# Performance work log

Hardware: AMD Instinct MI355X
Metric: run time of the kernel (lower is better)

Reference implementation:

```python
import jax, jax.numpy as jnp
import numpy as np
import math

D_MODEL = 512
N_HEADS = 8
D_K = D_MODEL // N_HEADS
N_SAMPLES = 16
BETA = 1.0
SCALE = 1.0 / math.sqrt(D_K)
PROPOSAL_TEMP = 0.5


def setup_inputs() -> dict:
    key = jax.random.key(0)
    ks = jax.random.split(key, 9)
    B, S = 2, 512
    x = jax.random.normal(ks[0], (B, S, D_MODEL), dtype=jnp.float32)
    init = lambda k: jax.random.normal(k, (D_MODEL, D_MODEL), dtype=jnp.float32) * 0.02
    return {
        "x": x,
        "Wq": init(ks[1]), "bq": jnp.zeros((D_MODEL,), jnp.float32),
        "Wk": init(ks[2]), "bk": jnp.zeros((D_MODEL,), jnp.float32),
        "Wv": init(ks[3]), "bv": jnp.zeros((D_MODEL,), jnp.float32),
        "Wo": init(ks[4]), "bo": jnp.zeros((D_MODEL,), jnp.float32),
    }


def _importance_sampled_weights(scores):
    # scores: [B,H,S,S]. Replicates the per-row Python loop, fully vectorized.
    B, H, Sq, Sk = scores.shape
    target = jax.nn.softmax(scores * BETA, axis=-1)            # [B,H,Sq,Sk]
    # optimal proposal: 0.5*target + 0.5*uniform
    prop = PROPOSAL_TEMP * target + (1.0 - PROPOSAL_TEMP) / Sk
    R = B * H * Sq
    tf = target.reshape(R, Sk)
    pf = prop.reshape(R, Sk)
    # tsu_backend.sample_binary_layer(log(p/(1-p))) == Bernoulli(p) sampling
    s = jax.random.bernoulli(jax.random.key(42), pf[:, None, :], (R, N_SAMPLES, Sk))
    # importance weight = prod(target[sel]) / (prod(prop[sel]) * prod(1-prop[~sel]))
    pt = jnp.prod(jnp.where(s, tf[:, None, :], 1.0), axis=-1)                 # [R,N]
    pp = jnp.prod(jnp.where(s, pf[:, None, :], 1.0 - pf[:, None, :]), axis=-1)
    valid = (s.sum(-1) > 0) & (pp > 0)
    w = jnp.where(valid, pt / jnp.maximum(pp, 1e-38), 0.0)
    ws = w.sum(-1, keepdims=True)
    w = jnp.where(ws > 0, w / jnp.maximum(ws, 1e-38), 1.0 / N_SAMPLES)        # [R,N]
    wa = jnp.einsum('rn,rnk->rk', w, s.astype(jnp.float32))                   # [R,Sk]
    was = wa.sum(-1, keepdims=True)
    wa = jnp.where(was > 0, wa / jnp.maximum(was, 1e-38), 1.0 / Sk)
    return wa.reshape(B, H, Sq, Sk)


def reference(x, Wq, bq, Wk, bk, Wv, bv, Wo, bo):
    B, S, Dm = x.shape
    proj = lambda W, b: (x @ W + b).reshape(B, S, N_HEADS, D_K).transpose(0, 2, 1, 3)
    Q = proj(Wq, bq)  # [B,H,S,dk]
    K = proj(Wk, bk)
    V = proj(Wv, bv)
    scores = jnp.einsum('bhqd,bhkd->bhqk', Q, K) * SCALE
    # torch builds weights via torch.tensor(...) which detaches => constant w.r.t. params
    attn = jax.lax.stop_gradient(_importance_sampled_weights(scores))
    out = jnp.einsum('bhqk,bhkd->bhqd', attn, V)
    out = out.transpose(0, 2, 1, 3).reshape(B, S, Dm)
    return out @ Wo + bo
```

## Files before the change

### kernel.cpp

```cpp
#include <hip/hip_runtime.h>
#include <cstdint>
#include <cstddef>


#define ROTL(x, r) __builtin_rotateleft32((x), (r))

#define QR8(s)                                                                \
  x0[0]+=x1[0];x0[1]+=x1[1];x0[2]+=x1[2];x0[3]+=x1[3];                        \
  x0[4]+=x1[4];x0[5]+=x1[5];x0[6]+=x1[6];x0[7]+=x1[7];                        \
  x1[0]=ROTL(x1[0],s);x1[1]=ROTL(x1[1],s);x1[2]=ROTL(x1[2],s);                \
  x1[3]=ROTL(x1[3],s);x1[4]=ROTL(x1[4],s);x1[5]=ROTL(x1[5],s);                \
  x1[6]=ROTL(x1[6],s);x1[7]=ROTL(x1[7],s);                                    \
  x1[0]^=x0[0];x1[1]^=x0[1];x1[2]^=x0[2];x1[3]^=x0[3];                        \
  x1[4]^=x0[4];x1[5]^=x0[5];x1[6]^=x0[6];x1[7]^=x0[7];
#define INJ8(X, Y)                                                            \
  x0[0]+=(X);x0[1]+=(X);x0[2]+=(X);x0[3]+=(X);                                \
  x0[4]+=(X);x0[5]+=(X);x0[6]+=(X);x0[7]+=(X);                                \
  x1[0]+=(Y);x1[1]+=(Y);x1[2]+=(Y);x1[3]+=(Y);                                \
  x1[4]+=(Y);x1[5]+=(Y);x1[6]+=(Y);x1[7]+=(Y);
#define INJ8Y(Y)                                                              \
  x1[0]+=(Y);x1[1]+=(Y);x1[2]+=(Y);x1[3]+=(Y);                                \
  x1[4]+=(Y);x1[5]+=(Y);x1[6]+=(Y);x1[7]+=(Y);

__global__ __launch_bounds__(256)
void qkv_gemm(const float* __restrict__ x,
              const float* __restrict__ Wq, const float* __restrict__ bq,
              const float* __restrict__ Wk, const float* __restrict__ bk,
              const float* __restrict__ Wv, const float* __restrict__ bv,
              const float* __restrict__ bo, float* __restrict__ outp,
              float* __restrict__ Qw, float* __restrict__ KTw,
              float* __restrict__ Vw) {
  const int tid = threadIdx.x;
  if (blockIdx.z == 3) {
    const int blk = blockIdx.y * 16 + blockIdx.x;
    const size_t base4 = (size_t)blk * 1024 + tid;
    const float4* bo4 = (const float4*)bo;
    float4* out4 = (float4*)outp;
#pragma unroll
    for (int i = 0; i < 4; ++i) {
      const size_t idx4 = base4 + (size_t)i * 256;
      out4[idx4] = bo4[idx4 & 127];
    }
    return;
  }
  const float* W; const float* bias;
  if (blockIdx.z == 0)      { W = Wq; bias = bq; }
  else if (blockIdx.z == 1) { W = Wk; bias = bk; }
  else                      { W = Wv; bias = bv; }

  __shared__ __align__(16) float smem[64 * 68];
  float (*At)[68] = (float(*)[68])smem;
  float (*Bs)[64] = (float(*)[64])(smem + 32 * 68);
  float (*T2)[68] = (float(*)[68])smem;

  const int tx = tid & 15, ty = tid >> 4;
  const int row0 = blockIdx.x * 64, col0 = blockIdx.y * 64;
  float acc[4][4] = {};

  const int ar = tid >> 2;
  const int kc0 = (tid & 3) << 3;
  const int br0 = tid >> 4,         bc0 = (tid & 15) << 2;
  const int br1 = (tid + 256) >> 4, bc1 = ((tid + 256) & 15) << 2;

  float4 aReg0, aReg1, bReg0, bReg1;
  {
    const int kk = 0;
    aReg0 = *(const float4*)&x[(size_t)(row0 + ar) * 512 + kk + kc0];
    aReg1 = *(const float4*)&x[(size_t)(row0 + ar) * 512 + kk + kc0 + 4];
    bReg0 = *(const float4*)&W[(size_t)(kk + br0) * 512 + col0 + bc0];
    bReg1 = *(const float4*)&W[(size_t)(kk + br1) * 512 + col0 + bc1];
  }

  for (int kk = 0; kk < 512; kk += 32) {
    At[kc0 + 0][ar] = aReg0.x; At[kc0 + 1][ar] = aReg0.y;
    At[kc0 + 2][ar] = aReg0.z; At[kc0 + 3][ar] = aReg0.w;
    At[kc0 + 4][ar] = aReg1.x; At[kc0 + 5][ar] = aReg1.y;
    At[kc0 + 6][ar] = aReg1.z; At[kc0 + 7][ar] = aReg1.w;
    *(float4*)&Bs[br0][bc0] = bReg0;
    *(float4*)&Bs[br1][bc1] = bReg1;
    __syncthreads();
    if (kk < 480) {
      const int kn = kk + 32;
      aReg0 = *(const float4*)&x[(size_t)(row0 + ar) * 512 + kn + kc0];
      aReg1 = *(const float4*)&x[(size_t)(row0 + ar) * 512 + kn + kc0 + 4];
      bReg0 = *(const float4*)&W[(size_t)(kn + br0) * 512 + col0 + bc0];
      bReg1 = *(const float4*)&W[(size_t)(kn + br1) * 512 + col0 + bc1];
    }
#pragma unroll
    for (int p = 0; p < 32; ++p) {
      const float4 a4 = *(const float4*)&At[p][ty << 2];
      const float4 b4 = *(const float4*)&Bs[p][tx << 2];
      acc[0][0] = fmaf(a4.x, b4.x, acc[0][0]); acc[0][1] = fmaf(a4.x, b4.y, acc[0][1]);
      acc[0][2] = fmaf(a4.x, b4.z, acc[0][2]); acc[0][3] = fmaf(a4.x, b4.w, acc[0][3]);
      acc[1][0] = fmaf(a4.y, b4.x, acc[1][0]); acc[1][1] = fmaf(a4.y, b4.y, acc[1][1]);
      acc[1][2] = fmaf(a4.y, b4.z, acc[1][2]); acc[1][3] = fmaf(a4.y, b4.w, acc[1][3]);
      acc[2][0] = fmaf(a4.z, b4.x, acc[2][0]); acc[2][1] = fmaf(a4.z, b4.y, acc[2][1]);
      acc[2][2] = fmaf(a4.z, b4.z, acc[2][2]); acc[2][3] = fmaf(a4.z, b4.w, acc[2][3]);
      acc[3][0] = fmaf(a4.w, b4.x, acc[3][0]); acc[3][1] = fmaf(a4.w, b4.y, acc[3][1]);
      acc[3][2] = fmaf(a4.w, b4.z, acc[3][2]); acc[3][3] = fmaf(a4.w, b4.w, acc[3][3]);
    }
    __syncthreads();
  }

  if (blockIdx.z == 0) {
#pragma unroll
    for (int i = 0; i < 4; ++i) {
      const int row = row0 + (ty << 2) + i;
      const int b = row >> 9, s = row & 511;
#pragma unroll
      for (int j = 0; j < 4; ++j) {
        const int col = col0 + (tx << 2) + j;
        const int h = col >> 6, d = col & 63;
        Qw[(((size_t)(b * 8 + h) * 512 + s) * 64) + d] = acc[i][j] + bias[col];
      }
    }
  } else if (blockIdx.z == 1) {
#pragma unroll
    for (int i = 0; i < 4; ++i) {
#pragma unroll
      for (int j = 0; j < 4; ++j) {
        const int col = col0 + (tx << 2) + j;
        T2[(tx << 2) + j][(ty << 2) + i] = acc[i][j] + bias[col];
      }
    }
    __syncthreads();
    const int c = tid >> 2, seg = tid & 3;
    const int b = row0 >> 9, h = blockIdx.y;
    const int s0 = (row0 & 511) + (seg << 4);
    float* dst = KTw + (((size_t)(b * 8 + h) * 64 + c) << 9) + s0;
#pragma unroll
    for (int i2 = 0; i2 < 4; ++i2) {
      *(float4*)&dst[i2 << 2] = *(const float4*)&T2[c][(seg << 4) + (i2 << 2)];
    }
  } else {
#pragma unroll
    for (int i = 0; i < 4; ++i) {
      const int row = row0 + (ty << 2) + i;
      const int b = row >> 9, s = row & 511;
#pragma unroll
      for (int j = 0; j < 4; ++j) {
        const int col = col0 + (tx << 2) + j;
        const int h = col >> 6, d = col & 63;
        Vw[(((size_t)(b * 8 + h) * 512 + s) * 64) + d] = acc[i][j] + bias[col];
      }
    }
  }
}

__global__ __launch_bounds__(256)
void fused_sample(const float* __restrict__ Q, const float* __restrict__ KT,
                  const float* __restrict__ V, const float* __restrict__ Wo,
                  float* __restrict__ outp) {
  const int bx = blockIdx.x;
  const int rbase = ((((bx & 7) << 8) | (bx >> 3)) << 2);
  const int bh = rbase >> 9, q0 = rbase & 511;
  const int b = rbase >> 12, h = (rbase >> 9) & 7;
  const int tid = threadIdx.x;

  __shared__ __align__(16) float qs[4][64];
  __shared__ __align__(16) float scs[4][512];
  __shared__ float red[8];
  __shared__ float redc[8];
  __shared__ float wr[16];
  __shared__ float tf[512];
  __shared__ __align__(16) uint32_t pscu2[512];
  __shared__ float wa[512];
  __shared__ float psum[4][64];
  __shared__ __align__(16) float o_s[4][64];
  __shared__ int   list[512];
  __shared__ int   cnt;

  qs[tid >> 6][tid & 63] =
      Q[((size_t)bh * 512 + q0 + (tid >> 6)) * 64 + (tid & 63)];
  __syncthreads();

  {
    const float* Kp = KT + (size_t)bh * 64 * 512 + tid;
    float s00 = 0.f, s01 = 0.f, s10 = 0.f, s11 = 0.f;
    float s20 = 0.f, s21 = 0.f, s30 = 0.f, s31 = 0.f;
#pragma unroll
    for (int d4 = 0; d4 < 16; ++d4) {
      float k0v[4], k1v[4];
#pragma unroll
      for (int j = 0; j < 4; ++j) {
        k0v[j] = Kp[(size_t)(d4 * 4 + j) * 512];
        k1v[j] = Kp[(size_t)(d4 * 4 + j) * 512 + 256];
      }
      const float4 q0v = *(const float4*)&qs[0][d4 << 2];
      const float4 q1v = *(const float4*)&qs[1][d4 << 2];
      const float4 q2v = *(const float4*)&qs[2][d4 << 2];
      const float4 q3v = *(const float4*)&qs[3][d4 << 2];
      s00 = fmaf(q0v.x, k0v[0], s00); s00 = fmaf(q0v.y, k0v[1], s00);
      s00 = fmaf(q0v.z, k0v[2], s00); s00 = fmaf(q0v.w, k0v[3], s00);
      s01 = fmaf(q0v.x, k1v[0], s01); s01 = fmaf(q0v.y, k1v[1], s01);
      s01 = fmaf(q0v.z, k1v[2], s01); s01 = fmaf(q0v.w, k1v[3], s01);
      s10 = fmaf(q1v.x, k0v[0], s10); s10 = fmaf(q1v.y, k0v[1], s10);
      s10 = fmaf(q1v.z, k0v[2], s10); s10 = fmaf(q1v.w, k0v[3], s10);
      s11 = fmaf(q1v.x, k1v[0], s11); s11 = fmaf(q1v.y, k1v[1], s11);
      s11 = fmaf(q1v.z, k1v[2], s11); s11 = fmaf(q1v.w, k1v[3], s11);
      s20 = fmaf(q2v.x, k0v[0], s20); s20 = fmaf(q2v.y, k0v[1], s20);
      s20 = fmaf(q2v.z, k0v[2], s20); s20 = fmaf(q2v.w, k0v[3], s20);
      s21 = fmaf(q2v.x, k1v[0], s21); s21 = fmaf(q2v.y, k1v[1], s21);
      s21 = fmaf(q2v.z, k1v[2], s21); s21 = fmaf(q2v.w, k1v[3], s21);
      s30 = fmaf(q3v.x, k0v[0], s30); s30 = fmaf(q3v.y, k0v[1], s30);
      s30 = fmaf(q3v.z, k0v[2], s30); s30 = fmaf(q3v.w, k0v[3], s30);
      s31 = fmaf(q3v.x, k1v[0], s31); s31 = fmaf(q3v.y, k1v[1], s31);
      s31 = fmaf(q3v.z, k1v[2], s31); s31 = fmaf(q3v.w, k1v[3], s31);
    }
    scs[0][tid] = s00 * 0.125f; scs[0][tid + 256] = s01 * 0.125f;
    scs[1][tid] = s10 * 0.125f; scs[1][tid + 256] = s11 * 0.125f;
    scs[2][tid] = s20 * 0.125f; scs[2][tid + 256] = s21 * 0.125f;
    scs[3][tid] = s30 * 0.125f; scs[3][tid + 256] = s31 * 0.125f;
  }

  const int n = tid >> 4, t = tid & 15;
  const int k0i = t << 5;
  const int g = tid >> 6, d = tid & 63;
  const float* Vb = V + ((size_t)(b * 8 + h) * 512) * 64;

  for (int rr = 0; rr < 4; ++rr) {
    const int r = rbase + rr;
    const float sc0 = scs[rr][tid];
    const float sc1 = scs[rr][tid + 256];

    float mx = fmaxf(sc0, sc1);
    for (int m = 1; m < 64; m <<= 1) mx = fmaxf(mx, __shfl_xor(mx, m));
    if ((tid & 63) == 0) red[tid >> 6] = mx;
    __syncthreads();
    const float rowmax = fmaxf(fmaxf(red[0], red[1]), fmaxf(red[2], red[3]));
    const float e0 = expf(sc0 - rowmax);
    const float e1 = expf(sc1 - rowmax);
    float ssum = e0 + e1;
    for (int m = 1; m < 64; m <<= 1) ssum += __shfl_xor(ssum, m);
    if ((tid & 63) == 0) red[4 + (tid >> 6)] = ssum;
    if (tid == 0) cnt = 0;
    __syncthreads();
    const float tot = red[4] + red[5] + red[6] + red[7];
    const float t0 = e0 / tot, t1 = e1 / tot;
    tf[tid] = t0; tf[tid + 256] = t1;
    wa[tid] = 0.f; wa[tid + 256] = 0.f;
    {
      const float p0 = fmaf(0.5f, t0, 0.0009765625f);
      const float p1 = fmaf(0.5f, t1, 0.0009765625f);
      {
        const int k = tid;
        pscu2[(((k & 31) >> 2) << 6) + ((k >> 5) << 2) + (k & 3)] =
            ((uint32_t)ceilf(p0 * 8388608.0f)) << 9;
      }
      {
        const int k = tid + 256;
        pscu2[(((k & 31) >> 2) << 6) + ((k >> 5) << 2) + (k & 3)] =
            ((uint32_t)ceilf(p1 * 8388608.0f)) << 9;
      }
      float ql = (1.f - p0) * (1.f - p1);
      for (int m = 1; m < 64; m <<= 1) ql *= __shfl_xor(ql, m);
      if ((tid & 63) == 0) redc[4 + (tid >> 6)] = ql;
    }
    __syncthreads();
    const float Qrow = redc[4] * redc[5] * redc[6] * redc[7];

    const uint32_t cbase =
        (uint32_t)r * 8192u + (uint32_t)n * 512u + (uint32_t)k0i + 42u;
    uint32_t bits = 0u;
#pragma unroll
    for (int jb = 0; jb < 32; jb += 8) {
      uint32_t x0[8], x1[8];
#pragma unroll
      for (int i = 0; i < 8; ++i) {
        const uint32_t c = cbase + (uint32_t)(jb + i);
        x0[i] = c;
        x1[i] = ROTL(c, 13) ^ c;
      }
      QR8(15) QR8(26) QR8(6)
      INJ8(42u, 0x1BD11BF1u)
      QR8(17) QR8(29) QR8(16) QR8(24)
      INJ8(0x1BD11BF0u, 2u)
      QR8(13) QR8(15) QR8(26) QR8(6)
      INJ8Y(45u)
      QR8(17) QR8(29) QR8(16) QR8(24)
      INJ8(42u, 0x1BD11BF4u)
      QR8(13) QR8(15) QR8(26) QR8(6)
      INJ8(0x1BD11BF0u, 5u)
      const uint4 pA = *(const uint4*)&pscu2[((jb >> 2) << 6) + (t << 2)];
      const uint4 pB = *(const uint4*)&pscu2[(((jb >> 2) + 1) << 6) + (t << 2)];
      bits |= (uint32_t)((x0[0] ^ x1[0]) < pA.x) << (jb + 0);
      bits |= (uint32_t)((x0[1] ^ x1[1]) < pA.y) << (jb + 1);
      bits |= (uint32_t)((x0[2] ^ x1[2]) < pA.z) << (jb + 2);
      bits |= (uint32_t)((x0[3] ^ x1[3]) < pA.w) << (jb + 3);
      bits |= (uint32_t)((x0[4] ^ x1[4]) < pB.x) << (jb + 4);
      bits |= (uint32_t)((x0[5] ^ x1[5]) < pB.y) << (jb + 5);
      bits |= (uint32_t)((x0[6] ^ x1[6]) < pB.z) << (jb + 6);
      bits |= (uint32_t)((x0[7] ^ x1[7]) < pB.w) << (jb + 7);
    }

    float ptl = 1.f, ratl = 1.f;
    int cl = __popc(bits);
    {
      uint32_t bb = bits;
      while (bb) {
        const int j = __builtin_ctz(bb);
        bb &= bb - 1u;
        const float tv = tf[k0i + j];
        const float p = fmaf(0.5f, tv, 0.0009765625f);
        ptl *= tv;
        ratl *= p / (1.f - p);
      }
    }
#pragma unroll
    for (int m = 1; m < 16; m <<= 1) {
      ptl *= __shfl_xor(ptl, m);
      ratl *= __shfl_xor(ratl, m);
      cl += __shfl_xor(cl, m);
    }
    if (t == 0) {
      const float pp = Qrow * ratl;
      wr[n] = (cl > 0 && pp > 0.f) ? (ptl / fmaxf(pp, 1e-38f)) : 0.f;
    }
    __syncthreads();
    float wsum = 0.f;
#pragma unroll
    for (int m2 = 0; m2 < 16; ++m2) wsum += wr[m2];
    const float wn = (wsum > 0.f) ? (wr[n] / fmaxf(wsum, 1e-38f)) : 0.0625f;
    {
      uint32_t bb = bits;
      while (bb) {
        const int j = __builtin_ctz(bb);
        bb &= bb - 1u;
        atomicAdd(&wa[k0i + j], wn);
      }
    }
    __syncthreads();

    float sp = wa[tid] + wa[tid + 256];
    for (int m = 1; m < 64; m <<= 1) sp += __shfl_xor(sp, m);
    if ((tid & 63) == 0) redc[tid >> 6] = sp;
    if (wa[tid] > 0.f)       { const int i = atomicAdd(&cnt, 1); list[i] = tid; }
    if (wa[tid + 256] > 0.f) { const int i = atomicAdd(&cnt, 1); list[i] = tid + 256; }
    __syncthreads();
    const float was = redc[0] + redc[1] + redc[2] + redc[3];
    const int nnz = cnt;

    float acc = 0.f;
    if (was > 0.f) {
      const float inv = 1.f / fmaxf(was, 1e-38f);
      for (int i = g; i < nnz; i += 4) {
        const int k = list[i];
        acc = fmaf(wa[k] * inv, Vb[(size_t)k * 64 + d], acc);
      }
    } else {
      for (int k = g; k < 512; k += 4) acc += Vb[(size_t)k * 64 + d];
      acc *= 0.001953125f;
    }
    psum[g][d] = acc;
    __syncthreads();
    if (g == 0)
      o_s[rr][d] = psum[0][d] + psum[1][d] + psum[2][d] + psum[3][d];
  }
  __syncthreads();

  {
    const float* Wh = Wo + ((size_t)h * 64) * 512;
    float a00 = 0.f, a01 = 0.f, a10 = 0.f, a11 = 0.f;
    float a20 = 0.f, a21 = 0.f, a30 = 0.f, a31 = 0.f;
#pragma unroll 8
    for (int dd = 0; dd < 64; ++dd) {
      const float w0 = Wh[(size_t)dd * 512 + tid];
      const float w1 = Wh[(size_t)dd * 512 + tid + 256];
      const float o0 = o_s[0][dd], o1 = o_s[1][dd];
      const float o2 = o_s[2][dd], o3 = o_s[3][dd];
      a00 = fmaf(o0, w0, a00); a01 = fmaf(o0, w1, a01);
      a10 = fmaf(o1, w0, a10); a11 = fmaf(o1, w1, a11);
      a20 = fmaf(o2, w0, a20); a21 = fmaf(o2, w1, a21);
      a30 = fmaf(o3, w0, a30); a31 = fmaf(o3, w1, a31);
    }
    float* orow = outp + ((size_t)(b * 512 + q0)) * 512;
    atomicAdd(&orow[tid], a00);         atomicAdd(&orow[tid + 256], a01);
    atomicAdd(&orow[512 + tid], a10);   atomicAdd(&orow[512 + tid + 256], a11);
    atomicAdd(&orow[1024 + tid], a20);  atomicAdd(&orow[1024 + tid + 256], a21);
    atomicAdd(&orow[1536 + tid], a30);  atomicAdd(&orow[1536 + tid + 256], a31);
  }
}

extern "C" void kernel_launch(void* const* d_in, const int* in_sizes, int n_in,
                              void* d_out, int out_size, void* d_ws,
                              size_t ws_size, hipStream_t stream) {
  const float* x  = (const float*)d_in[0];
  const float* Wq = (const float*)d_in[1];
  const float* bq = (const float*)d_in[2];
  const float* Wk = (const float*)d_in[3];
  const float* bk = (const float*)d_in[4];
  const float* Wv = (const float*)d_in[5];
  const float* bv = (const float*)d_in[6];
  const float* Wo = (const float*)d_in[7];
  const float* bo = (const float*)d_in[8];
  float* out = (float*)d_out;

  float* ws = (float*)d_ws;
  float* Qw = ws;
  float* KT = ws + 524288;
  float* Vw = ws + 1048576;

  dim3 gq(16, 8, 4);
  qkv_gemm<<<gq, 256, 0, stream>>>(x, Wq, bq, Wk, bk, Wv, bv, bo, out,
                                   Qw, KT, Vw);
  fused_sample<<<2048, 256, 0, stream>>>(Qw, KT, Vw, Wo, out);
}
```

Baseline: 247.8 us.

## Halve QKV GEMM row tile and double-buffer shared memory tiles

The QKV projection GEMM now uses 32-row tiles instead of 64, doubling the grid to 1024 blocks for better occupancy across CUs. Shared memory A/B tiles are double-buffered so the next tile is stored while the current one is consumed, removing one barrier per k-step. Each thread now computes a 2x4 output block, which lowers arithmetic intensity per shared load. The bias-broadcast init blocks and K-transpose epilogue are adjusted to the new tile shape.

```diff
diff --git a/kernel.cpp b/kernel.cpp
--- a/kernel.cpp
+++ b/kernel.cpp
@@ -32,15 +32,12 @@
               float* __restrict__ Vw) {
   const int tid = threadIdx.x;
   if (blockIdx.z == 3) {
-    const int blk = blockIdx.y * 16 + blockIdx.x;
-    const size_t base4 = (size_t)blk * 1024 + tid;
+    const int blk = blockIdx.y * 32 + blockIdx.x;
+    const size_t base4 = (size_t)blk * 512 + tid;
     const float4* bo4 = (const float4*)bo;
     float4* out4 = (float4*)outp;
-#pragma unroll
-    for (int i = 0; i < 4; ++i) {
-      const size_t idx4 = base4 + (size_t)i * 256;
-      out4[idx4] = bo4[idx4 & 127];
-    }
+    out4[base4] = bo4[base4 & 127];
+    out4[base4 + 256] = bo4[(base4 + 256) & 127];
     return;
   }
   const float* W; const float* bias;
@@ -48,101 +45,95 @@
   else if (blockIdx.z == 1) { W = Wk; bias = bk; }
   else                      { W = Wv; bias = bv; }
 
-  __shared__ __align__(16) float smem[64 * 68];
-  float (*At)[68] = (float(*)[68])smem;
-  float (*Bs)[64] = (float(*)[64])(smem + 32 * 68);
-  float (*T2)[68] = (float(*)[68])smem;
+  __shared__ __align__(16) float smem[2 * (32 * 34 + 32 * 64)];
+  float (*At0)[34] = (float(*)[34])smem;
+  float (*Bs0)[64] = (float(*)[64])(smem + 32 * 34);
+  float (*At1)[34] = (float(*)[34])(smem + 3136);
+  float (*Bs1)[64] = (float(*)[64])(smem + 3136 + 32 * 34);
+  float (*T2)[34]  = (float(*)[34])smem;
 
   const int tx = tid & 15, ty = tid >> 4;
-  const int row0 = blockIdx.x * 64, col0 = blockIdx.y * 64;
-  float acc[4][4] = {};
-
-  const int ar = tid >> 2;
-  const int kc0 = (tid & 3) << 3;
+  const int row0 = blockIdx.x * 32, col0 = blockIdx.y * 64;
+  float acc[2][4] = {};
+
+  const int ar = tid >> 3;
+  const int kc = (tid & 7) << 2;
   const int br0 = tid >> 4,         bc0 = (tid & 15) << 2;
   const int br1 = (tid + 256) >> 4, bc1 = ((tid + 256) & 15) << 2;
 
-  float4 aReg0, aReg1, bReg0, bReg1;
-  {
-    const int kk = 0;
-    aReg0 = *(const float4*)&x[(size_t)(row0 + ar) * 512 + kk + kc0];
-    aReg1 = *(const float4*)&x[(size_t)(row0 + ar) * 512 + kk + kc0 + 4];
-    bReg0 = *(const float4*)&W[(size_t)(kk + br0) * 512 + col0 + bc0];
-    bReg1 = *(const float4*)&W[(size_t)(kk + br1) * 512 + col0 + bc1];
-  }
+  float4 aR, bR0, bR1;
+  aR  = *(const float4*)&x[(size_t)(row0 + ar) * 512 + kc];
+  bR0 = *(const float4*)&W[(size_t)br0 * 512 + col0 + bc0];
+  bR1 = *(const float4*)&W[(size_t)br1 * 512 + col0 + bc1];
+
+  At0[kc + 0][ar] = aR.x; At0[kc + 1][ar] = aR.y;
+  At0[kc + 2][ar] = aR.z; At0[kc + 3][ar] = aR.w;
+  *(float4*)&Bs0[br0][bc0] = bR0;
+  *(float4*)&Bs0[br1][bc1] = bR1;
+  __syncthreads();
+
+  float (*Atc)[34] = At0; float (*Bsc)[64] = Bs0;
+  float (*Atn)[34] = At1; float (*Bsn)[64] = Bs1;
 
   for (int kk = 0; kk < 512; kk += 32) {
-    At[kc0 + 0][ar] = aReg0.x; At[kc0 + 1][ar] = aReg0.y;
-    At[kc0 + 2][ar] = aReg0.z; At[kc0 + 3][ar] = aReg0.w;
-    At[kc0 + 4][ar] = aReg1.x; At[kc0 + 5][ar] = aReg1.y;
-    At[kc0 + 6][ar] = aReg1.z; At[kc0 + 7][ar] = aReg1.w;
-    *(float4*)&Bs[br0][bc0] = bReg0;
-    *(float4*)&Bs[br1][bc1] = bReg1;
-    __syncthreads();
     if (kk < 480) {
       const int kn = kk + 32;
-      aReg0 = *(const float4*)&x[(size_t)(row0 + ar) * 512 + kn + kc0];
-      aReg1 = *(const float4*)&x[(size_t)(row0 + ar) * 512 + kn + kc0 + 4];
-      bReg0 = *(const float4*)&W[(size_t)(kn + br0) * 512 + col0 + bc0];
-      bReg1 = *(const float4*)&W[(size_t)(kn + br1) * 512 + col0 + bc1];
+      aR  = *(const float4*)&x[(size_t)(row0 + ar) * 512 + kn + kc];
+      bR0 = *(const float4*)&W[(size_t)(kn + br0) * 512 + col0 + bc0];
+      bR1 = *(const float4*)&W[(size_t)(kn + br1) * 512 + col0 + bc1];
     }
 #pragma unroll
     for (int p = 0; p < 32; ++p) {
-      const float4 a4 = *(const float4*)&At[p][ty << 2];
-      const float4 b4 = *(const float4*)&Bs[p][tx << 2];
-      acc[0][0] = fmaf(a4.x, b4.x, acc[0][0]); acc[0][1] = fmaf(a4.x, b4.y, acc[0][1]);
-      acc[0][2] = fmaf(a4.x, b4.z, acc[0][2]); acc[0][3] = fmaf(a4.x, b4.w, acc[0][3]);
-      acc[1][0] = fmaf(a4.y, b4.x, acc[1][0]); acc[1][1] = fmaf(a4.y, b4.y, acc[1][1]);
-      acc[1][2] = fmaf(a4.y, b4.z, acc[1][2]); acc[1][3] = fmaf(a4.y, b4.w, acc[1][3]);
-      acc[2][0] = fmaf(a4.z, b4.x, acc[2][0]); acc[2][1] = fmaf(a4.z, b4.y, acc[2][1]);
-      acc[2][2] = fmaf(a4.z, b4.z, acc[2][2]); acc[2][3] = fmaf(a4.z, b4.w, acc[2][3]);
-      acc[3][0] = fmaf(a4.w, b4.x, acc[3][0]); acc[3][1] = fmaf(a4.w, b4.y, acc[3][1]);
-      acc[3][2] = fmaf(a4.w, b4.z, acc[3][2]); acc[3][3] = fmaf(a4.w, b4.w, acc[3][3]);
-    }
-    __syncthreads();
-  }
-
-  if (blockIdx.z == 0) {
-#pragma unroll
-    for (int i = 0; i < 4; ++i) {
-      const int row = row0 + (ty << 2) + i;
+      const float2 a2 = *(const float2*)&Atc[p][ty << 1];
+      const float4 b4 = *(const float4*)&Bsc[p][tx << 2];
+      acc[0][0] = fmaf(a2.x, b4.x, acc[0][0]); acc[0][1] = fmaf(a2.x, b4.y, acc[0][1]);
+      acc[0][2] = fmaf(a2.x, b4.z, acc[0][2]); acc[0][3] = fmaf(a2.x, b4.w, acc[0][3]);
+      acc[1][0] = fmaf(a2.y, b4.x, acc[1][0]); acc[1][1] = fmaf(a2.y, b4.y, acc[1][1]);
+      acc[1][2] = fmaf(a2.y, b4.z, acc[1][2]); acc[1][3] = fmaf(a2.y, b4.w, acc[1][3]);
+    }
+    if (kk < 480) {
+      Atn[kc + 0][ar] = aR.x; Atn[kc + 1][ar] = aR.y;
+      Atn[kc + 2][ar] = aR.z; Atn[kc + 3][ar] = aR.w;
+      *(float4*)&Bsn[br0][bc0] = bR0;
+      *(float4*)&Bsn[br1][bc1] = bR1;
+    }
+    __syncthreads();
+    float (*tA)[34] = Atc; Atc = Atn; Atn = tA;
+    float (*tB)[64] = Bsc; Bsc = Bsn; Bsn = tB;
+  }
+
+  const int h = blockIdx.y;
+  if (blockIdx.z == 0 || blockIdx.z == 2) {
+    float* dst = (blockIdx.z == 0) ? Qw : Vw;
+#pragma unroll
+    for (int i = 0; i < 2; ++i) {
+      const int row = row0 + (ty << 1) + i;
       const int b = row >> 9, s = row & 511;
 #pragma unroll
       for (int j = 0; j < 4; ++j) {
         const int col = col0 + (tx << 2) + j;
-        const int h = col >> 6, d = col & 63;
-        Qw[(((size_t)(b * 8 + h) * 512 + s) * 64) + d] = acc[i][j] + bias[col];
-      }
-    }
-  } else if (blockIdx.z == 1) {
-#pragma unroll
-    for (int i = 0; i < 4; ++i) {
+        const int d = col & 63;
+        dst[(((size_t)(b * 8 + h) * 512 + s) * 64) + d] = acc[i][j] + bias[col];
+      }
+    }
+  } else {
+#pragma unroll
+    for (int i = 0; i < 2; ++i) {
 #pragma unroll
       for (int j = 0; j < 4; ++j) {
         const int col = col0 + (tx << 2) + j;
-        T2[(tx << 2) + j][(ty << 2) + i] = acc[i][j] + bias[col];
-      }
-    }
-    __syncthreads();
-    const int c = tid >> 2, seg = tid & 3;
-    const int b = row0 >> 9, h = blockIdx.y;
-    const int s0 = (row0 & 511) + (seg << 4);
-    float* dst = KTw + (((size_t)(b * 8 + h) * 64 + c) << 9) + s0;
-#pragma unroll
-    for (int i2 = 0; i2 < 4; ++i2) {
-      *(float4*)&dst[i2 << 2] = *(const float4*)&T2[c][(seg << 4) + (i2 << 2)];
-    }
-  } else {
-#pragma unroll
-    for (int i = 0; i < 4; ++i) {
-      const int row = row0 + (ty << 2) + i;
-      const int b = row >> 9, s = row & 511;
-#pragma unroll
-      for (int j = 0; j < 4; ++j) {
-        const int col = col0 + (tx << 2) + j;
-        const int h = col >> 6, d = col & 63;
-        Vw[(((size_t)(b * 8 + h) * 512 + s) * 64) + d] = acc[i][j] + bias[col];
-      }
+        T2[(tx << 2) + j][(ty << 1) + i] = acc[i][j] + bias[col];
+      }
+    }
+    __syncthreads();
+    const int b = row0 >> 9;
+    const int s0 = row0 & 511;
+#pragma unroll
+    for (int i2 = 0; i2 < 2; ++i2) {
+      const int idx = tid + (i2 << 8);
+      const int c = idx >> 3, seg = idx & 7;
+      float* dst = KTw + (((size_t)(b * 8 + h) * 64 + c) << 9) + s0 + (seg << 2);
+      *(float4*)dst = *(const float4*)&T2[c][seg << 2];
     }
   }
 }
@@ -400,7 +391,7 @@
   float* KT = ws + 524288;
   float* Vw = ws + 1048576;
 
-  dim3 gq(16, 8, 4);
+  dim3 gq(32, 8, 4);
   qkv_gemm<<<gq, 256, 0, stream>>>(x, Wq, bq, Wk, bk, Wv, bv, bo, out,
                                    Qw, KT, Vw);
   fused_sample<<<2048, 256, 0, stream>>>(Qw, KT, Vw, Wo, out);
```

Measured after the change: 252.4 us. About the same (+1.9%).
